# Optimization experiments

Hardware: AMD Instinct MI355X
Metric: run time of the kernel (lower is better)

## Reference

```python
import jax, jax.numpy as jnp
import numpy as np

N_NODES = 100_000
N_EDGES = 1_600_000
N_FEAT = 64
E_FEAT = 32
OUT_FEAT = 64


def _xavier_normal(key, shape, gain):
    fan_out, fan_in = shape
    std = gain * np.sqrt(2.0 / (fan_in + fan_out))
    return jax.random.normal(key, shape, dtype=jnp.float32) * std


def setup_inputs() -> dict:
    key = jax.random.key(0)
    ks = jax.random.split(key, 9)
    d_cat = 2 * N_FEAT + E_FEAT  # 160
    n_feat = jax.random.normal(ks[0], (N_NODES, N_FEAT), dtype=jnp.float32)
    e_feat = jax.random.normal(ks[1], (N_EDGES, E_FEAT), dtype=jnp.float32)
    src = jax.random.randint(ks[2], (N_EDGES,), 0, N_NODES, dtype=jnp.int32)
    dst = jax.random.randint(ks[3], (N_EDGES,), 0, N_NODES, dtype=jnp.int32)
    gain = np.sqrt(2.0)
    bound_msg = 1.0 / np.sqrt(d_cat)
    return {
        "n_feat": n_feat,
        "e_feat": e_feat,
        "src": src,
        "dst": dst,
        # W_msg uses default torch Linear init (kaiming-uniform-ish); exact init irrelevant for correctness
        "W_msg_w": jax.random.uniform(ks[4], (OUT_FEAT, d_cat), jnp.float32, -bound_msg, bound_msg),
        "W_msg_b": jax.random.uniform(ks[5], (OUT_FEAT,), jnp.float32, -bound_msg, bound_msg),
        # W uses xavier_normal with gain sqrt(2)
        "W_w": _xavier_normal(ks[6], (2 * OUT_FEAT, d_cat), gain),
        "W_b": jax.random.uniform(ks[7], (2 * OUT_FEAT,), jnp.float32, -bound_msg, bound_msg),
        "a": _xavier_normal(ks[8], (2 * OUT_FEAT, 1), gain),
    }


def reference(n_feat, e_feat, src, dst, W_msg_w, W_msg_b, W_w, W_b, a):
    # gather: per-edge concat [E, 2*n_feat + e_feat]
    feat_cat = jnp.concatenate([n_feat[src], n_feat[dst], e_feat], axis=1)
    # edge attention logits: leaky_relu((feat_cat @ W^T + b) @ a)  -> [E]
    w_feat = feat_cat @ W_w.T + W_b                      # [E, 2*out_feat]
    logits = jax.nn.leaky_relu(w_feat @ a[:, 0])         # [E]
    # edge softmax grouped by destination node
    seg_max = jax.ops.segment_max(logits, dst, num_segments=N_NODES)  # [N]
    ex = jnp.exp(logits - seg_max[dst])                  # [E]
    seg_sum = jax.ops.segment_sum(ex, dst, num_segments=N_NODES)     # [N]
    att = ex / seg_sum[dst]                              # [E]
    # messages and weighted scatter-sum aggregation
    msg = feat_cat @ W_msg_w.T + W_msg_b                 # [E, out_feat]
    agg = jax.ops.segment_sum(att[:, None] * msg, dst, num_segments=N_NODES)  # [N, out_feat]
    return jax.nn.relu(agg)
```

## Files before the change

kernel.cpp:

```cpp
#include <hip/hip_runtime.h>
#include <hip/hip_bf16.h>
#include <hip/hip_fp16.h>

#define N_NODES 100000
#define N_EDGES 1600000
#define NF 64
#define EF 32

#define SCAN_B 512
#define SCAN_NB ((N_NODES + SCAN_B - 1) / SCAN_B)
#define CNT_NB ((N_EDGES + 255) / 256)
#define K1_NB ((N_NODES + 511) / 512)


__device__ __forceinline__ unsigned pkh2(float a, float b) {
  __half2 h = __floats2half2_rn(a, b);
  return *reinterpret_cast<unsigned*>(&h);
}

__global__ __launch_bounds__(256) void kA_count_prep(
    const int* __restrict__ dst, int* __restrict__ cnt, int* __restrict__ rank,
    const float* __restrict__ Ww, const float* __restrict__ Wb,
    const float* __restrict__ a, const float* __restrict__ Wmsg,
    float* __restrict__ v, float* __restrict__ W1T, float* __restrict__ W2T,
    float* __restrict__ WmeT) {
  int b = blockIdx.x;
  int t = threadIdx.x;
  if (b < CNT_NB) {
    int e = b * 256 + t;
    if (e < N_EDGES) rank[e] = atomicAdd(&cnt[dst[e]], 1);
    return;
  }
  for (int j = t; j < 160; j += 256) {
    float s = 0.f;
    for (int k = 0; k < 128; ++k) s = fmaf(a[k], Ww[k * 160 + j], s);
    v[j] = s;
  }
  if (t == 0) {
    float s = 0.f;
    for (int k = 0; k < 128; ++k) s = fmaf(a[k], Wb[k], s);
    v[160] = s;
  }
  for (int idx = t; idx < 64 * 64; idx += 256) {
    int j = idx >> 6, i = idx & 63;
    W1T[idx] = Wmsg[i * 160 + j];
    W2T[idx] = Wmsg[i * 160 + 64 + j];
  }
  for (int idx = t; idx < 32 * 64; idx += 256) {
    int j = idx >> 6, i = idx & 63;
    WmeT[idx] = Wmsg[i * 160 + 128 + j];
  }
}

__global__ __launch_bounds__(512) void kB_scan1_node(
    const int* __restrict__ cnt, int* __restrict__ bsum,
    const float* __restrict__ nf_g, const float* __restrict__ v,
    const float* __restrict__ W1T, const float* __restrict__ W2T,
    float* __restrict__ s1, float* __restrict__ s2,
    __half* __restrict__ m_src_h, float* __restrict__ m_dst) {
  __shared__ int sh[SCAN_B];
  int t = threadIdx.x;
  if (blockIdx.x < SCAN_NB) {
    int i = blockIdx.x * SCAN_B + t;
    sh[t] = (i < N_NODES) ? cnt[i] : 0;
    __syncthreads();
    for (int d = SCAN_B / 2; d > 0; d >>= 1) {
      if (t < d) sh[t] += sh[t + d];
      __syncthreads();
    }
    if (t == 0) bsum[blockIdx.x] = sh[0];
    return;
  }
  int n = (blockIdx.x - SCAN_NB) * 512 + t;
  if (n >= N_NODES) return;
  const float4* nf4 = (const float4*)(nf_g + (size_t)n * NF);
  float acc[64];
#pragma unroll
  for (int i = 0; i < 64; ++i) acc[i] = 0.f;
  float s1a = 0.f, s2a = 0.f;
  for (int j4 = 0; j4 < 16; ++j4) {
    float4 q = nf4[j4];
    float xs[4] = {q.x, q.y, q.z, q.w};
#pragma unroll
    for (int u = 0; u < 4; ++u) {
      int j = j4 * 4 + u;
      float x = xs[u];
      s1a = fmaf(v[j], x, s1a);
      s2a = fmaf(v[64 + j], x, s2a);
      const float* w = W1T + j * 64;
#pragma unroll
      for (int i = 0; i < 64; ++i) acc[i] = fmaf(w[i], x, acc[i]);
    }
  }
  s1[n] = s1a;
  s2[n] = s2a;
  uint4* ms4 = (uint4*)(m_src_h + (size_t)n * NF);
#pragma unroll
  for (int b = 0; b < 8; ++b)
    ms4[b] = make_uint4(pkh2(acc[b * 8 + 0], acc[b * 8 + 1]),
                        pkh2(acc[b * 8 + 2], acc[b * 8 + 3]),
                        pkh2(acc[b * 8 + 4], acc[b * 8 + 5]),
                        pkh2(acc[b * 8 + 6], acc[b * 8 + 7]));
#pragma unroll
  for (int i = 0; i < 64; ++i) acc[i] = 0.f;
  for (int j4 = 0; j4 < 16; ++j4) {
    float4 q = nf4[j4];
    float xs[4] = {q.x, q.y, q.z, q.w};
#pragma unroll
    for (int u = 0; u < 4; ++u) {
      int j = j4 * 4 + u;
      float x = xs[u];
      const float* w = W2T + j * 64;
#pragma unroll
      for (int i = 0; i < 64; ++i) acc[i] = fmaf(w[i], x, acc[i]);
    }
  }
  float* md = m_dst + (size_t)n * NF;
#pragma unroll
  for (int i = 0; i < 64; ++i) md[i] = acc[i];
}

__global__ __launch_bounds__(256) void kS2(const int* __restrict__ bsum,
                                           int* __restrict__ boff,
                                           int* __restrict__ row_ptr) {
  __shared__ int sh[256];
  int t = threadIdx.x;
  sh[t] = (t < SCAN_NB) ? bsum[t] : 0;
  __syncthreads();
  for (int d = 1; d < 256; d <<= 1) {
    int val = (t >= d) ? sh[t - d] : 0;
    __syncthreads();
    sh[t] += val;
    __syncthreads();
  }
  if (t < SCAN_NB) boff[t] = (t == 0) ? 0 : sh[t - 1];
  if (t == 255) row_ptr[N_NODES] = sh[255];
}

__global__ __launch_bounds__(SCAN_B) void kS3(const int* __restrict__ cnt,
                                              const int* __restrict__ boff,
                                              int* __restrict__ row_ptr) {
  __shared__ int sh[SCAN_B];
  int t = threadIdx.x;
  int i = blockIdx.x * SCAN_B + t;
  int val = (i < N_NODES) ? cnt[i] : 0;
  sh[t] = val;
  __syncthreads();
  for (int d = 1; d < SCAN_B; d <<= 1) {
    int u = (t >= d) ? sh[t - d] : 0;
    __syncthreads();
    sh[t] += u;
    __syncthreads();
  }
  if (i < N_NODES) row_ptr[i] = boff[blockIdx.x] + sh[t] - val;
}

__global__ __launch_bounds__(256) void kE_scatter(
    const int* __restrict__ src, const int* __restrict__ dst,
    const int* __restrict__ rank, const int* __restrict__ row_ptr,
    const float* __restrict__ e_feat, uint4* __restrict__ ef_s4) {
  int e = blockIdx.x * 256 + threadIdx.x;
  if (e >= N_EDGES) return;
  unsigned sn = (unsigned)src[e];
  int dn = dst[e];
  int rk = rank[e];
  const float4* efr = (const float4*)(e_feat + (size_t)e * EF);
  float4 q[8];
#pragma unroll
  for (int i = 0; i < 8; ++i) q[i] = efr[i];
  int p = row_ptr[dn] + rk;
  unsigned u[16];
#pragma unroll
  for (int i = 0; i < 8; ++i) {
    u[2 * i] = pkh2(q[i].x, q[i].y);
    u[2 * i + 1] = pkh2(q[i].z, q[i].w);
  }
#pragma unroll
  for (int j = 0; j < 16; ++j)
    u[j] = (u[j] & ~1u) | ((sn >> j) & 1u);
  u[0] = (u[0] & ~0x10000u) | (((sn >> 16) & 1u) << 16);
  uint4* o = ef_s4 + (size_t)p * 4;
  o[0] = make_uint4(u[0], u[1], u[2], u[3]);
  o[1] = make_uint4(u[4], u[5], u[6], u[7]);
  o[2] = make_uint4(u[8], u[9], u[10], u[11]);
  o[3] = make_uint4(u[12], u[13], u[14], u[15]);
}

__global__ __launch_bounds__(256) void k3_agg(
    const int* __restrict__ row_ptr, const unsigned* __restrict__ efu,
    const __half* __restrict__ m_src_h, const float* __restrict__ s1,
    const float* __restrict__ s2, const float* __restrict__ v,
    const float* __restrict__ m_dst, const float* __restrict__ WmeT,
    const float* __restrict__ Wmsg_b, float* __restrict__ out) {
  int lane = threadIdx.x & 63;
  int wid = threadIdx.x >> 6;
  int n = blockIdx.x * 4 + wid;
  if (n >= N_NODES) return;
  int start = row_ptr[n];
  int end = row_ptr[n + 1];
  int g = lane >> 4;
  int c2 = lane & 15;
  float vlo = v[128 + 2 * c2];
  float vhi = v[128 + 2 * c2 + 1];
  float cbias = v[160];
  float s2n = s2[n];
  float sum_ex = 0.f, acc_ms = 0.f;
  float aefx = 0.f, aefy = 0.f;
  if (start < end) {
    unsigned ucur = efu[(size_t)min(start + g, N_EDGES - 1) * 16 + c2];
    unsigned unxt = efu[(size_t)min(start + 4 + g, N_EDGES - 1) * 16 + c2];
    unsigned long long b0 = __ballot((int)(ucur & 1u));
    unsigned long long b1 = __ballot((int)(ucur & 0x10000u));
    int a0 = min((int)((b0 >> 0) & 0xFFFF) | ((int)((b1 >> 0) & 1) << 16),
                 N_NODES - 1);
    int a1 = min((int)((b0 >> 16) & 0xFFFF) | ((int)((b1 >> 16) & 1) << 16),
                 N_NODES - 1);
    int a2 = min((int)((b0 >> 32) & 0xFFFF) | ((int)((b1 >> 32) & 1) << 16),
                 N_NODES - 1);
    int a3 = min((int)((b0 >> 48) & 0xFFFF) | ((int)((b1 >> 48) & 1) << 16),
                 N_NODES - 1);
    int sgA = (g < 2) ? (g ? a1 : a0) : ((g == 2) ? a2 : a3);
    float s1A = s1[sgA];
    __half hA0 = m_src_h[(size_t)a0 * NF + lane];
    __half hA1 = m_src_h[(size_t)a1 * NF + lane];
    __half hA2 = m_src_h[(size_t)a2 * NF + lane];
    __half hA3 = m_src_h[(size_t)a3 * NF + lane];
    for (int k = start; k < end; k += 4) {
      unsigned ufar = efu[(size_t)min(k + 8 + g, N_EDGES - 1) * 16 + c2];
      unsigned long long c0 = __ballot((int)(unxt & 1u));
      unsigned long long c1 = __ballot((int)(unxt & 0x10000u));
      int e0 = min((int)((c0 >> 0) & 0xFFFF) | ((int)((c1 >> 0) & 1) << 16),
                   N_NODES - 1);
      int e1 = min((int)((c0 >> 16) & 0xFFFF) | ((int)((c1 >> 16) & 1) << 16),
                   N_NODES - 1);
      int e2 = min((int)((c0 >> 32) & 0xFFFF) | ((int)((c1 >> 32) & 1) << 16),
                   N_NODES - 1);
      int e3 = min((int)((c0 >> 48) & 0xFFFF) | ((int)((c1 >> 48) & 1) << 16),
                   N_NODES - 1);
      int sgB = (g < 2) ? (g ? e1 : e0) : ((g == 2) ? e2 : e3);
      float s1B = s1[sgB];
      __half hB0 = m_src_h[(size_t)e0 * NF + lane];
      __half hB1 = m_src_h[(size_t)e1 * NF + lane];
      __half hB2 = m_src_h[(size_t)e2 * NF + lane];
      __half hB3 = m_src_h[(size_t)e3 * NF + lane];
      __half2 h2 = *reinterpret_cast<__half2*>(&ucur);
      float2 ef2 = __half22float2(h2);
      float pt = fmaf(ef2.y, vhi, ef2.x * vlo);
      pt += __shfl_xor(pt, 1);
      pt += __shfl_xor(pt, 2);
      pt += __shfl_xor(pt, 4);
      pt += __shfl_xor(pt, 8);
      float lg = s1A + s2n + pt + cbias;
      float l = lg > 0.f ? lg : 0.01f * lg;
      float exv = ((k + g) < end) ? __expf(l) : 0.f;
      aefx = fmaf(exv, ef2.x, aefx);
      aefy = fmaf(exv, ef2.y, aefy);
      float ex0 = __shfl(exv, 0);
      float ex1 = __shfl(exv, 16);
      float ex2 = __shfl(exv, 32);
      float ex3 = __shfl(exv, 48);
      sum_ex += (ex0 + ex1) + (ex2 + ex3);
      acc_ms = fmaf(ex0, __half2float(hA0), acc_ms);
      acc_ms = fmaf(ex1, __half2float(hA1), acc_ms);
      acc_ms = fmaf(ex2, __half2float(hA2), acc_ms);
      acc_ms = fmaf(ex3, __half2float(hA3), acc_ms);
      ucur = unxt;
      unxt = ufar;
      hA0 = hB0; hA1 = hB1; hA2 = hB2; hA3 = hB3;
      s1A = s1B;
    }
  }
  aefx += __shfl_xor(aefx, 16);
  aefx += __shfl_xor(aefx, 32);
  aefy += __shfl_xor(aefy, 16);
  aefy += __shfl_xor(aefy, 32);
  float mm = 0.f;
#pragma unroll
  for (int jp = 0; jp < 16; ++jp) {
    float ea = __shfl(aefx, jp);
    float eb = __shfl(aefy, jp);
    mm = fmaf(WmeT[(2 * jp) * 64 + lane], ea, mm);
    mm = fmaf(WmeT[(2 * jp + 1) * 64 + lane], eb, mm);
  }
  float o = 0.f;
  if (sum_ex > 0.f) {
    o = (acc_ms + mm) / sum_ex + m_dst[(size_t)n * NF + lane] + Wmsg_b[lane];
    o = fmaxf(o, 0.f);
  }
  out[(size_t)n * NF + lane] = o;
}

extern "C" void kernel_launch(void* const* d_in, const int* in_sizes, int n_in,
                              void* d_out, int out_size, void* d_ws,
                              size_t ws_size, hipStream_t stream) {
  const float* n_feat = (const float*)d_in[0];
  const float* e_feat = (const float*)d_in[1];
  const int* src = (const int*)d_in[2];
  const int* dst = (const int*)d_in[3];
  const float* Wmsg_w = (const float*)d_in[4];
  const float* Wmsg_b = (const float*)d_in[5];
  const float* W_w = (const float*)d_in[6];
  const float* W_b = (const float*)d_in[7];
  const float* a = (const float*)d_in[8];
  float* out = (float*)d_out;

  char* ws = (char*)d_ws;
  size_t off = 0;
  auto alloc = [&](size_t bytes) -> char* {
    char* p = ws + off;
    off = (off + bytes + 255) & ~(size_t)255;
    return p;
  };
  float* v = (float*)alloc(161 * 4);
  float* W1T = (float*)alloc(64 * 64 * 4);
  float* W2T = (float*)alloc(64 * 64 * 4);
  float* WmeT = (float*)alloc(32 * 64 * 4);
  float* s1 = (float*)alloc(N_NODES * 4);
  float* s2 = (float*)alloc(N_NODES * 4);
  __half* m_src_h = (__half*)alloc((size_t)N_NODES * NF * 2);
  float* m_dst = (float*)alloc((size_t)N_NODES * NF * 4);
  int* cnt = (int*)alloc(N_NODES * 4);
  int* row_ptr = (int*)alloc((N_NODES + 1) * 4);
  int* rank = (int*)alloc((size_t)N_EDGES * 4);
  int* bsum = (int*)alloc(SCAN_NB * 4);
  int* boff = (int*)alloc(SCAN_NB * 4);
  __half* ef_s = (__half*)alloc(((size_t)N_EDGES + 8) * EF * 2);
  if (off > ws_size) return;

  hipMemsetAsync(cnt, 0, N_NODES * 4, stream);
  kA_count_prep<<<CNT_NB + 1, 256, 0, stream>>>(dst, cnt, rank, W_w, W_b, a,
                                                Wmsg_w, v, W1T, W2T, WmeT);
  kB_scan1_node<<<SCAN_NB + K1_NB, 512, 0, stream>>>(
      cnt, bsum, n_feat, v, W1T, W2T, s1, s2, m_src_h, m_dst);
  kS2<<<1, 256, 0, stream>>>(bsum, boff, row_ptr);
  kS3<<<SCAN_NB, SCAN_B, 0, stream>>>(cnt, boff, row_ptr);
  kE_scatter<<<(N_EDGES + 255) / 256, 256, 0, stream>>>(
      src, dst, rank, row_ptr, e_feat, (uint4*)ef_s);
  k3_agg<<<(N_NODES + 3) / 4, 256, 0, stream>>>(
      row_ptr, (const unsigned*)ef_s, m_src_h, s1, s2, v, m_dst, WmeT,
      Wmsg_b, out);
}
```

Before: 584.8 us.

## Compute edge logits in scatter pass, embed in fp16 pad bits, fuse scans

Moves the per-edge attention logit computation (edge-feature dot product, s1/s2 lookups, leaky relu) from the aggregation kernel into the scatter kernel. The fp16 logit is packed into spare low mantissa bits of the stored edge features, and the aggregator recovers it with an extra ballot. This removes the shuffle reduction and the s1 gather from the hot aggregation loop. It also replaces the per-edge rank array with an atomic cursor and fuses the two scan kernels into one that redundantly scans block sums in every block. Costs are extra atomics in scatter, nondeterministic edge order within a segment, and fp16 logit precision.

```diff
diff --git a/kernel.cpp b/kernel.cpp
--- a/kernel.cpp
+++ b/kernel.cpp
@@ -19,7 +19,7 @@
 }
 
 __global__ __launch_bounds__(256) void kA_count_prep(
-    const int* __restrict__ dst, int* __restrict__ cnt, int* __restrict__ rank,
+    const int* __restrict__ dst, int* __restrict__ cnt,
     const float* __restrict__ Ww, const float* __restrict__ Wb,
     const float* __restrict__ a, const float* __restrict__ Wmsg,
     float* __restrict__ v, float* __restrict__ W1T, float* __restrict__ W2T,
@@ -28,7 +28,7 @@
   int t = threadIdx.x;
   if (b < CNT_NB) {
     int e = b * 256 + t;
-    if (e < N_EDGES) rank[e] = atomicAdd(&cnt[dst[e]], 1);
+    if (e < N_EDGES) atomicAdd(&cnt[dst[e]], 1);
     return;
   }
   for (int j = t; j < 160; j += 256) {
@@ -120,28 +120,23 @@
   for (int i = 0; i < 64; ++i) md[i] = acc[i];
 }
 
-__global__ __launch_bounds__(256) void kS2(const int* __restrict__ bsum,
-                                           int* __restrict__ boff,
-                                           int* __restrict__ row_ptr) {
-  __shared__ int sh[256];
+__global__ __launch_bounds__(SCAN_B) void kS23(const int* __restrict__ cnt,
+                                               const int* __restrict__ bsum,
+                                               int* __restrict__ row_ptr,
+                                               int* __restrict__ cursor) {
+  __shared__ int sb[256];
+  __shared__ int sh[SCAN_B];
   int t = threadIdx.x;
-  sh[t] = (t < SCAN_NB) ? bsum[t] : 0;
+  if (t < 256) sb[t] = (t < SCAN_NB) ? bsum[t] : 0;
   __syncthreads();
   for (int d = 1; d < 256; d <<= 1) {
-    int val = (t >= d) ? sh[t - d] : 0;
-    __syncthreads();
-    sh[t] += val;
-    __syncthreads();
-  }
-  if (t < SCAN_NB) boff[t] = (t == 0) ? 0 : sh[t - 1];
-  if (t == 255) row_ptr[N_NODES] = sh[255];
-}
-
-__global__ __launch_bounds__(SCAN_B) void kS3(const int* __restrict__ cnt,
-                                              const int* __restrict__ boff,
-                                              int* __restrict__ row_ptr) {
-  __shared__ int sh[SCAN_B];
-  int t = threadIdx.x;
+    int val = 0;
+    if (t < 256 && t >= d) val = sb[t - d];
+    __syncthreads();
+    if (t < 256) sb[t] += val;
+    __syncthreads();
+  }
+  int boff = (blockIdx.x == 0) ? 0 : sb[blockIdx.x - 1];
   int i = blockIdx.x * SCAN_B + t;
   int val = (i < N_NODES) ? cnt[i] : 0;
   sh[t] = val;
@@ -152,23 +147,39 @@
     sh[t] += u;
     __syncthreads();
   }
-  if (i < N_NODES) row_ptr[i] = boff[blockIdx.x] + sh[t] - val;
+  if (i < N_NODES) {
+    int excl = boff + sh[t] - val;
+    row_ptr[i] = excl;
+    cursor[i] = excl;
+  }
+  if (blockIdx.x == 0 && t == 0) row_ptr[N_NODES] = sb[SCAN_NB - 1];
 }
 
 __global__ __launch_bounds__(256) void kE_scatter(
     const int* __restrict__ src, const int* __restrict__ dst,
-    const int* __restrict__ rank, const int* __restrict__ row_ptr,
-    const float* __restrict__ e_feat, uint4* __restrict__ ef_s4) {
+    const float* __restrict__ e_feat, const float* __restrict__ s1,
+    const float* __restrict__ s2, const float* __restrict__ v,
+    int* __restrict__ cursor, uint4* __restrict__ ef_s4) {
   int e = blockIdx.x * 256 + threadIdx.x;
   if (e >= N_EDGES) return;
   unsigned sn = (unsigned)src[e];
   int dn = dst[e];
-  int rk = rank[e];
   const float4* efr = (const float4*)(e_feat + (size_t)e * EF);
   float4 q[8];
 #pragma unroll
   for (int i = 0; i < 8; ++i) q[i] = efr[i];
-  int p = row_ptr[dn] + rk;
+  float t = 0.f;
+#pragma unroll
+  for (int i = 0; i < 8; ++i) {
+    t = fmaf(q[i].x, v[128 + i * 4 + 0], t);
+    t = fmaf(q[i].y, v[128 + i * 4 + 1], t);
+    t = fmaf(q[i].z, v[128 + i * 4 + 2], t);
+    t = fmaf(q[i].w, v[128 + i * 4 + 3], t);
+  }
+  float lg = s1[sn] + s2[dn] + t + v[160];
+  float l = lg > 0.f ? lg : 0.01f * lg;
+  unsigned lh = (unsigned)__half_as_ushort(__float2half_rn(l));
+  int p = atomicAdd(&cursor[dn], 1);
   unsigned u[16];
 #pragma unroll
   for (int i = 0; i < 8; ++i) {
@@ -178,7 +189,11 @@
 #pragma unroll
   for (int j = 0; j < 16; ++j)
     u[j] = (u[j] & ~1u) | ((sn >> j) & 1u);
-  u[0] = (u[0] & ~0x10000u) | (((sn >> 16) & 1u) << 16);
+#pragma unroll
+  for (int j = 1; j < 16; ++j)
+    u[j] = (u[j] & ~0x10000u) | (((lh >> (j - 1)) & 1u) << 16);
+  u[0] = (u[0] & ~0x10002u) | (((sn >> 16) & 1u) << 16) |
+         (((lh >> 15) & 1u) << 1);
   uint4* o = ef_s4 + (size_t)p * 4;
   o[0] = make_uint4(u[0], u[1], u[2], u[3]);
   o[1] = make_uint4(u[4], u[5], u[6], u[7]);
@@ -188,10 +203,9 @@
 
 __global__ __launch_bounds__(256) void k3_agg(
     const int* __restrict__ row_ptr, const unsigned* __restrict__ efu,
-    const __half* __restrict__ m_src_h, const float* __restrict__ s1,
-    const float* __restrict__ s2, const float* __restrict__ v,
-    const float* __restrict__ m_dst, const float* __restrict__ WmeT,
-    const float* __restrict__ Wmsg_b, float* __restrict__ out) {
+    const __half* __restrict__ m_src_h, const float* __restrict__ m_dst,
+    const float* __restrict__ WmeT, const float* __restrict__ Wmsg_b,
+    float* __restrict__ out) {
   int lane = threadIdx.x & 63;
   int wid = threadIdx.x >> 6;
   int n = blockIdx.x * 4 + wid;
@@ -199,75 +213,67 @@
   int start = row_ptr[n];
   int end = row_ptr[n + 1];
   int g = lane >> 4;
-  int c2 = lane & 15;
-  float vlo = v[128 + 2 * c2];
-  float vhi = v[128 + 2 * c2 + 1];
-  float cbias = v[160];
-  float s2n = s2[n];
+  int w = lane & 15;
   float sum_ex = 0.f, acc_ms = 0.f;
   float aefx = 0.f, aefy = 0.f;
   if (start < end) {
-    unsigned ucur = efu[(size_t)min(start + g, N_EDGES - 1) * 16 + c2];
-    unsigned unxt = efu[(size_t)min(start + 4 + g, N_EDGES - 1) * 16 + c2];
+    unsigned ucur = efu[(size_t)min(start + g, N_EDGES - 1) * 16 + w];
+    unsigned unxt = efu[(size_t)min(start + 4 + g, N_EDGES - 1) * 16 + w];
     unsigned long long b0 = __ballot((int)(ucur & 1u));
     unsigned long long b1 = __ballot((int)(ucur & 0x10000u));
-    int a0 = min((int)((b0 >> 0) & 0xFFFF) | ((int)((b1 >> 0) & 1) << 16),
-                 N_NODES - 1);
-    int a1 = min((int)((b0 >> 16) & 0xFFFF) | ((int)((b1 >> 16) & 1) << 16),
-                 N_NODES - 1);
-    int a2 = min((int)((b0 >> 32) & 0xFFFF) | ((int)((b1 >> 32) & 1) << 16),
-                 N_NODES - 1);
-    int a3 = min((int)((b0 >> 48) & 0xFFFF) | ((int)((b1 >> 48) & 1) << 16),
-                 N_NODES - 1);
-    int sgA = (g < 2) ? (g ? a1 : a0) : ((g == 2) ? a2 : a3);
-    float s1A = s1[sgA];
-    __half hA0 = m_src_h[(size_t)a0 * NF + lane];
-    __half hA1 = m_src_h[(size_t)a1 * NF + lane];
-    __half hA2 = m_src_h[(size_t)a2 * NF + lane];
-    __half hA3 = m_src_h[(size_t)a3 * NF + lane];
+    unsigned long long b2 = __ballot((int)(ucur & 2u));
+    float lA[4];
+    __half hA[4];
+#pragma unroll
+    for (int gg = 0; gg < 4; ++gg) {
+      int sh16 = gg << 4;
+      int s = (int)((b0 >> sh16) & 0xFFFFull) |
+              ((int)((b1 >> sh16) & 1ull) << 16);
+      s = min(s, N_NODES - 1);
+      unsigned lb = (unsigned)((b1 >> (sh16 + 1)) & 0x7FFFull) |
+                    ((unsigned)((b2 >> sh16) & 1ull) << 15);
+      lA[gg] = __half2float(__ushort_as_half((unsigned short)lb));
+      hA[gg] = m_src_h[(size_t)s * NF + lane];
+    }
     for (int k = start; k < end; k += 4) {
-      unsigned ufar = efu[(size_t)min(k + 8 + g, N_EDGES - 1) * 16 + c2];
+      unsigned ufar = efu[(size_t)min(k + 8 + g, N_EDGES - 1) * 16 + w];
       unsigned long long c0 = __ballot((int)(unxt & 1u));
       unsigned long long c1 = __ballot((int)(unxt & 0x10000u));
-      int e0 = min((int)((c0 >> 0) & 0xFFFF) | ((int)((c1 >> 0) & 1) << 16),
-                   N_NODES - 1);
-      int e1 = min((int)((c0 >> 16) & 0xFFFF) | ((int)((c1 >> 16) & 1) << 16),
-                   N_NODES - 1);
-      int e2 = min((int)((c0 >> 32) & 0xFFFF) | ((int)((c1 >> 32) & 1) << 16),
-                   N_NODES - 1);
-      int e3 = min((int)((c0 >> 48) & 0xFFFF) | ((int)((c1 >> 48) & 1) << 16),
-                   N_NODES - 1);
-      int sgB = (g < 2) ? (g ? e1 : e0) : ((g == 2) ? e2 : e3);
-      float s1B = s1[sgB];
-      __half hB0 = m_src_h[(size_t)e0 * NF + lane];
-      __half hB1 = m_src_h[(size_t)e1 * NF + lane];
-      __half hB2 = m_src_h[(size_t)e2 * NF + lane];
-      __half hB3 = m_src_h[(size_t)e3 * NF + lane];
+      unsigned long long c2m = __ballot((int)(unxt & 2u));
+      float lB[4];
+      __half hB[4];
+#pragma unroll
+      for (int gg = 0; gg < 4; ++gg) {
+        int sh16 = gg << 4;
+        int s = (int)((c0 >> sh16) & 0xFFFFull) |
+                ((int)((c1 >> sh16) & 1ull) << 16);
+        s = min(s, N_NODES - 1);
+        unsigned lb = (unsigned)((c1 >> (sh16 + 1)) & 0x7FFFull) |
+                      ((unsigned)((c2m >> sh16) & 1ull) << 15);
+        lB[gg] = __half2float(__ushort_as_half((unsigned short)lb));
+        hB[gg] = m_src_h[(size_t)s * NF + lane];
+      }
+      float e0 = (k + 0 < end) ? __expf(lA[0]) : 0.f;
+      float e1 = (k + 1 < end) ? __expf(lA[1]) : 0.f;
+      float e2 = (k + 2 < end) ? __expf(lA[2]) : 0.f;
+      float e3 = (k + 3 < end) ? __expf(lA[3]) : 0.f;
       __half2 h2 = *reinterpret_cast<__half2*>(&ucur);
       float2 ef2 = __half22float2(h2);
-      float pt = fmaf(ef2.y, vhi, ef2.x * vlo);
-      pt += __shfl_xor(pt, 1);
-      pt += __shfl_xor(pt, 2);
-      pt += __shfl_xor(pt, 4);
-      pt += __shfl_xor(pt, 8);
-      float lg = s1A + s2n + pt + cbias;
-      float l = lg > 0.f ? lg : 0.01f * lg;
-      float exv = ((k + g) < end) ? __expf(l) : 0.f;
-      aefx = fmaf(exv, ef2.x, aefx);
-      aefy = fmaf(exv, ef2.y, aefy);
-      float ex0 = __shfl(exv, 0);
-      float ex1 = __shfl(exv, 16);
-      float ex2 = __shfl(exv, 32);
-      float ex3 = __shfl(exv, 48);
-      sum_ex += (ex0 + ex1) + (ex2 + ex3);
-      acc_ms = fmaf(ex0, __half2float(hA0), acc_ms);
-      acc_ms = fmaf(ex1, __half2float(hA1), acc_ms);
-      acc_ms = fmaf(ex2, __half2float(hA2), acc_ms);
-      acc_ms = fmaf(ex3, __half2float(hA3), acc_ms);
+      float eg = (g == 0) ? e0 : (g == 1) ? e1 : (g == 2) ? e2 : e3;
+      aefx = fmaf(eg, ef2.x, aefx);
+      aefy = fmaf(eg, ef2.y, aefy);
+      sum_ex += (e0 + e1) + (e2 + e3);
+      acc_ms = fmaf(e0, __half2float(hA[0]), acc_ms);
+      acc_ms = fmaf(e1, __half2float(hA[1]), acc_ms);
+      acc_ms = fmaf(e2, __half2float(hA[2]), acc_ms);
+      acc_ms = fmaf(e3, __half2float(hA[3]), acc_ms);
       ucur = unxt;
       unxt = ufar;
-      hA0 = hB0; hA1 = hB1; hA2 = hB2; hA3 = hB3;
-      s1A = s1B;
+#pragma unroll
+      for (int gg = 0; gg < 4; ++gg) {
+        lA[gg] = lB[gg];
+        hA[gg] = hB[gg];
+      }
     }
   }
   aefx += __shfl_xor(aefx, 16);
@@ -321,22 +327,19 @@
   float* m_dst = (float*)alloc((size_t)N_NODES * NF * 4);
   int* cnt = (int*)alloc(N_NODES * 4);
   int* row_ptr = (int*)alloc((N_NODES + 1) * 4);
-  int* rank = (int*)alloc((size_t)N_EDGES * 4);
+  int* cursor = (int*)alloc(N_NODES * 4);
   int* bsum = (int*)alloc(SCAN_NB * 4);
-  int* boff = (int*)alloc(SCAN_NB * 4);
   __half* ef_s = (__half*)alloc(((size_t)N_EDGES + 8) * EF * 2);
   if (off > ws_size) return;
 
   hipMemsetAsync(cnt, 0, N_NODES * 4, stream);
-  kA_count_prep<<<CNT_NB + 1, 256, 0, stream>>>(dst, cnt, rank, W_w, W_b, a,
+  kA_count_prep<<<CNT_NB + 1, 256, 0, stream>>>(dst, cnt, W_w, W_b, a,
                                                 Wmsg_w, v, W1T, W2T, WmeT);
   kB_scan1_node<<<SCAN_NB + K1_NB, 512, 0, stream>>>(
       cnt, bsum, n_feat, v, W1T, W2T, s1, s2, m_src_h, m_dst);
-  kS2<<<1, 256, 0, stream>>>(bsum, boff, row_ptr);
-  kS3<<<SCAN_NB, SCAN_B, 0, stream>>>(cnt, boff, row_ptr);
+  kS23<<<SCAN_NB, SCAN_B, 0, stream>>>(cnt, bsum, row_ptr, cursor);
   kE_scatter<<<(N_EDGES + 255) / 256, 256, 0, stream>>>(
-      src, dst, rank, row_ptr, e_feat, (uint4*)ef_s);
+      src, dst, e_feat, s1, s2, v, cursor, (uint4*)ef_s);
   k3_agg<<<(N_NODES + 3) / 4, 256, 0, stream>>>(
-      row_ptr, (const unsigned*)ef_s, m_src_h, s1, s2, v, m_dst, WmeT,
-      Wmsg_b, out);
-}
+      row_ptr, (const unsigned*)ef_s, m_src_h, m_dst, WmeT, Wmsg_b, out);
+}
```

After: 602.2 us. 1.03x slower.
